# Kernel optimization log

Measured on AMD Instinct MI355X. Metric: run time of the kernel, lower is better.

The kernel has to match this reference:

```python
import jax, jax.numpy as jnp
import numpy as np

B, H, S, F, D = 16, 8, 512, 512, 64
RANK = 12
TOPK_RATIO = 0.1
LN_EPS = 1e-5


def _layernorm(x, w, b):
    mu = jnp.mean(x, axis=-1, keepdims=True)
    var = jnp.mean((x - mu) ** 2, axis=-1, keepdims=True)
    return (x - mu) * jax.lax.rsqrt(var + LN_EPS) * w + b


def _topk_mask(logits, k):
    # keep top-k along last axis, set the rest to -inf (torch topk+scatter equivalent)
    vals, _ = jax.lax.top_k(logits, k)
    kth = vals[..., -1:]
    return jnp.where(logits >= kth, logits, -jnp.inf)


def setup_inputs() -> dict:
    key = jax.random.key(0)
    ks = jax.random.split(key, 4)
    values = jax.random.normal(ks[0], (B, F, H, D), dtype=jnp.float32)
    # stand-in for per-head orthogonal init (rows ~ unit norm scale)
    alpha = jax.random.normal(ks[1], (H, S, F), dtype=jnp.float32) / np.float32(np.sqrt(F))
    temp = jnp.ones((H, 1), dtype=jnp.float32)
    gamma_hs = jnp.zeros((H, S, 1), dtype=jnp.float32)
    U = jax.random.normal(ks[2], (H, S, RANK), dtype=jnp.float32) * 0.01
    V = jax.random.normal(ks[3], (H, RANK, F), dtype=jnp.float32) * 0.01
    ln_w = jnp.ones((F,), dtype=jnp.float32)
    ln_b = jnp.zeros((F,), dtype=jnp.float32)
    return {"values": values, "alpha": alpha, "temp": temp, "gamma_hs": gamma_hs,
            "U": U, "V": V, "ln_w": ln_w, "ln_b": ln_b}


def reference(values, alpha, temp, gamma_hs, U, V, ln_w, ln_b):
    scale = np.float32(1.0 / np.sqrt(F))
    alpha_logits = (alpha * scale)[None]                      # [1,H,S,F]

    # data logits from value energies
    w = jnp.transpose(values, (0, 2, 1, 3))                    # [B,H,F,D]
    energy = jnp.mean(w * w, axis=-1)                          # [B,H,F]
    rms = jnp.maximum(jnp.sqrt(jnp.mean(energy, axis=-1, keepdims=True)), 1e-6)
    score = energy / rms                                       # [B,H,F]
    gain = jax.nn.softplus(temp)[:, 0]                         # [H]
    score = score * gain[None, :, None]
    score = _layernorm(score, ln_w, ln_b)                      # LN over F
    bilinear = jnp.einsum('hsr,hrf->hsf', U, V)                # [H,S,F]
    data_logits = score[:, :, None, :] + gamma_hs[None] + bilinear[None]  # [B,H,S,F]

    k = max(1, int(TOPK_RATIO * F))
    data_logits = _topk_mask(data_logits, k)
    alpha_logits = _topk_mask(alpha_logits, k)

    attn_mix = jax.nn.softmax(data_logits, axis=-1) + jax.nn.softmax(alpha_logits, axis=-1)
    out = jnp.einsum('bhsf,bfhd->bshd', attn_mix, values)      # [B,S,H,D]
    return out
```

## Files before the change

kernel.cpp:

```cpp
#include <hip/hip_runtime.h>
#include <math.h>

#define BB 16
#define HH 8
#define SS 512
#define FF 512
#define DD 64
#define RANKK 12
#define KTOP 51
#define ROWS 8

typedef __attribute__((ext_vector_type(8))) short bf16x8;
typedef __attribute__((ext_vector_type(4))) float f32x4;

__device__ __forceinline__ unsigned short f2bf(float x){
  unsigned u = __float_as_uint(x);
  return (unsigned short)((u + 0x7FFFu + ((u>>16)&1u)) >> 16);
}
__device__ __forceinline__ float bf2f(unsigned short h){
  return __uint_as_float(((unsigned)h)<<16);
}

__device__ __forceinline__ unsigned f2ord(float x){
  unsigned u = __float_as_uint(x);
  return (u & 0x80000000u) ? ~u : (u | 0x80000000u);
}

__device__ __forceinline__ void topk_softmax8(float (&a)[8]){
  unsigned key[8];
#pragma unroll
  for (int j=0;j<8;++j) key[j] = f2ord(a[j]);
  unsigned T = 0u;
#pragma unroll
  for (int bit=31; bit>=0; --bit){
    unsigned Tp = T | (1u<<bit);
    int cnt = 0;
#pragma unroll
    for (int j=0;j<8;++j){
      unsigned long long bl = __ballot(key[j] >= Tp);
      cnt += __popcll(bl);
    }
    if (cnt >= KTOP) T = Tp;
    if (cnt == KTOP) break;
  }
  float m = a[0];
#pragma unroll
  for (int j=1;j<8;++j) m = fmaxf(m, a[j]);
#pragma unroll
  for (int off=32; off>=1; off>>=1) m = fmaxf(m, __shfl_xor(m, off));
  float sum = 0.f;
#pragma unroll
  for (int j=0;j<8;++j){
    float e = (key[j] >= T) ? expf(a[j]-m) : 0.f;
    a[j] = e; sum += e;
  }
#pragma unroll
  for (int off=32; off>=1; off>>=1) sum += __shfl_xor(sum, off);
  float inv = 1.f/sum;
#pragma unroll
  for (int j=0;j<8;++j) a[j] *= inv;
}

__global__ __launch_bounds__(512) void k_prep_all(
    const float* __restrict__ values, const float* __restrict__ temp,
    const float* __restrict__ ln_w, const float* __restrict__ ln_b,
    const float* __restrict__ alpha, float* __restrict__ score_ln,
    unsigned short* __restrict__ hiP, unsigned short* __restrict__ loP,
    float* __restrict__ A_soft)
{
  const int tid = threadIdx.x, w = tid >> 6, lane = tid & 63;
  if (blockIdx.x >= BB*HH){
    const int row = (int)(blockIdx.x - BB*HH) * ROWS + w;
    const float SCALE = (float)(1.0/sqrt((double)FF));
    const float* ar = alpha + (size_t)row*FF + lane*8;
    float4 v0 = *(const float4*)ar;
    float4 v1 = *(const float4*)(ar+4);
    float a[8] = {v0.x*SCALE, v0.y*SCALE, v0.z*SCALE, v0.w*SCALE,
                  v1.x*SCALE, v1.y*SCALE, v1.z*SCALE, v1.w*SCALE};
    topk_softmax8(a);
    float* orow = A_soft + (size_t)row*FF + lane*8;
    *(float4*)orow     = make_float4(a[0],a[1],a[2],a[3]);
    *(float4*)(orow+4) = make_float4(a[4],a[5],a[6],a[7]);
    return;
  }
  __shared__ float tile[64][65];
  __shared__ float s_e[FF];
  __shared__ float ps[8], ps2[8];
  const int b = blockIdx.x / HH, h = blockIdx.x % HH;
  const float* vb = values + ((size_t)b*FF*HH + h)*DD;

  for (int c=0;c<8;++c){
#pragma unroll
    for (int p=0;p<8;++p){
      const int fi = p*8 + w;
      const int f  = c*64 + fi;
      tile[fi][lane] = vb[(size_t)f*HH*DD + lane];
    }
    __syncthreads();
    {
      const int d  = w*8 + (lane>>3);
      const int fj = (lane&7)*8;
      unsigned short hs[8], ls[8];
#pragma unroll
      for (int j=0;j<8;++j){
        float x = tile[fj+j][d];
        hs[j] = f2bf(x);
        ls[j] = f2bf(x - bf2f(hs[j]));
      }
      uint4 H4, L4;
      H4.x=(unsigned)hs[0]|((unsigned)hs[1]<<16); H4.y=(unsigned)hs[2]|((unsigned)hs[3]<<16);
      H4.z=(unsigned)hs[4]|((unsigned)hs[5]<<16); H4.w=(unsigned)hs[6]|((unsigned)hs[7]<<16);
      L4.x=(unsigned)ls[0]|((unsigned)ls[1]<<16); L4.y=(unsigned)ls[2]|((unsigned)ls[3]<<16);
      L4.z=(unsigned)ls[4]|((unsigned)ls[5]<<16); L4.w=(unsigned)ls[6]|((unsigned)ls[7]<<16);
      const size_t base = ((size_t)blockIdx.x*DD + d)*FF + c*64 + fj;
      *(uint4*)(hiP + base) = H4;
      *(uint4*)(loP + base) = L4;
    }
    __syncthreads();
  }

  for (int i=0;i<FF/8;++i){
    int f = w*(FF/8) + i;
    float v = vb[(size_t)f*HH*DD + lane];
    float e = v*v;
#pragma unroll
    for (int off=32; off>=1; off>>=1) e += __shfl_xor(e, off);
    if (lane==0) s_e[f] = e * (1.0f/DD);
  }
  __syncthreads();
  float e = s_e[tid];
  float se = e, se2 = e*e;
#pragma unroll
  for (int off=32; off>=1; off>>=1){ se += __shfl_xor(se, off); se2 += __shfl_xor(se2, off); }
  if (lane==0){ ps[w]=se; ps2[w]=se2; }
  __syncthreads();
  float S1=0.f, S2=0.f;
#pragma unroll
  for (int g=0; g<8; ++g){ S1 += ps[g]; S2 += ps2[g]; }
  float meanE = S1 * (1.0f/FF);
  float rms = fmaxf(sqrtf(meanE), 1e-6f);
  float t = temp[h];
  float gain = (t > 20.f) ? t : log1pf(expf(t));
  float c = gain / rms;
  float mu = c * meanE;
  float var = c*c*(S2*(1.0f/FF) - meanE*meanE);
  float inv = rsqrtf(var + 1e-5f);
  score_ln[(size_t)blockIdx.x*FF + tid] = (c*e - mu)*inv*ln_w[tid] + ln_b[tid];
}

__global__ __launch_bounds__(512) void k_score(const float* __restrict__ values,
    const float* __restrict__ temp, const float* __restrict__ ln_w,
    const float* __restrict__ ln_b, float* __restrict__ score_ln)
{
  const int b = blockIdx.x / HH, h = blockIdx.x % HH;
  const int tid = threadIdx.x, w = tid >> 6, lane = tid & 63;
  __shared__ float s_e[FF];
  __shared__ float ps[8], ps2[8];
  const float* vb = values + ((size_t)b*FF*HH + h)*DD;
  for (int i=0;i<FF/8;++i){
    int f = w*(FF/8) + i;
    float v = vb[(size_t)f*HH*DD + lane];
    float e = v*v;
#pragma unroll
    for (int off=32; off>=1; off>>=1) e += __shfl_xor(e, off);
    if (lane==0) s_e[f] = e * (1.0f/DD);
  }
  __syncthreads();
  float e = s_e[tid];
  float se = e, se2 = e*e;
#pragma unroll
  for (int off=32; off>=1; off>>=1){ se += __shfl_xor(se, off); se2 += __shfl_xor(se2, off); }
  if (lane==0){ ps[w]=se; ps2[w]=se2; }
  __syncthreads();
  float S1=0.f, S2=0.f;
#pragma unroll
  for (int g=0; g<8; ++g){ S1 += ps[g]; S2 += ps2[g]; }
  float meanE = S1 * (1.0f/FF);
  float rms = fmaxf(sqrtf(meanE), 1e-6f);
  float t = temp[h];
  float gain = (t > 20.f) ? t : log1pf(expf(t));
  float c = gain / rms;
  float mu = c * meanE;
  float var = c*c*(S2*(1.0f/FF) - meanE*meanE);
  float inv = rsqrtf(var + 1e-5f);
  score_ln[(size_t)blockIdx.x*FF + tid] = (c*e - mu)*inv*ln_w[tid] + ln_b[tid];
}

__global__ __launch_bounds__(512) void k_alpha(const float* __restrict__ alpha,
                                               float* __restrict__ A_soft)
{
  const int w = threadIdx.x >> 6, lane = threadIdx.x & 63;
  const int row = blockIdx.x * ROWS + w;
  const float SCALE = (float)(1.0/sqrt((double)FF));
  const float* ar = alpha + (size_t)row*FF + lane*8;
  float4 v0 = *(const float4*)ar;
  float4 v1 = *(const float4*)(ar+4);
  float a[8] = {v0.x*SCALE, v0.y*SCALE, v0.z*SCALE, v0.w*SCALE,
                v1.x*SCALE, v1.y*SCALE, v1.z*SCALE, v1.w*SCALE};
  topk_softmax8(a);
  float* orow = A_soft + (size_t)row*FF + lane*8;
  *(float4*)orow     = make_float4(a[0],a[1],a[2],a[3]);
  *(float4*)(orow+4) = make_float4(a[4],a[5],a[6],a[7]);
}

__global__ __launch_bounds__(512) void k_prep_t(const float* __restrict__ values,
    unsigned short* __restrict__ hiP, unsigned short* __restrict__ loP, int b0)
{
  const int bloc_h = blockIdx.x;
  const int b = b0 + bloc_h / HH, h = bloc_h % HH;
  const int tid = threadIdx.x, w = tid >> 6, lane = tid & 63;
  __shared__ float tile[64][65];
  const float* vb = values + ((size_t)b*FF*HH + h)*DD;
  for (int c=0;c<8;++c){
#pragma unroll
    for (int p=0;p<8;++p){
      const int fi = p*8 + w;
      const int f  = c*64 + fi;
      tile[fi][lane] = vb[(size_t)f*HH*DD + lane];
    }
    __syncthreads();
    {
      const int d  = w*8 + (lane>>3);
      const int fj = (lane&7)*8;
      unsigned short hs[8], ls[8];
#pragma unroll
      for (int j=0;j<8;++j){
        float x = tile[fj+j][d];
        hs[j] = f2bf(x);
        ls[j] = f2bf(x - bf2f(hs[j]));
      }
      uint4 H4, L4;
      H4.x=(unsigned)hs[0]|((unsigned)hs[1]<<16); H4.y=(unsigned)hs[2]|((unsigned)hs[3]<<16);
      H4.z=(unsigned)hs[4]|((unsigned)hs[5]<<16); H4.w=(unsigned)hs[6]|((unsigned)hs[7]<<16);
      L4.x=(unsigned)ls[0]|((unsigned)ls[1]<<16); L4.y=(unsigned)ls[2]|((unsigned)ls[3]<<16);
      L4.z=(unsigned)ls[4]|((unsigned)ls[5]<<16); L4.w=(unsigned)ls[6]|((unsigned)ls[7]<<16);
      const size_t base = ((size_t)bloc_h*DD + d)*FF + c*64 + fj;
      *(uint4*)(hiP + base) = H4;
      *(uint4*)(loP + base) = L4;
    }
    __syncthreads();
  }
}

__device__ __forceinline__ void build_mix_row(int bh, int h, int s, int lane,
    const float* __restrict__ score_ln, const float* __restrict__ gamma,
    const float* __restrict__ U, const float* __restrict__ V,
    const float* __restrict__ A_soft, float4& m0, float4& m1)
{
  const int f0 = lane*8;
  const float* sr = score_ln + (size_t)bh*FF + f0;
  float4 sv0 = *(const float4*)sr;
  float4 sv1 = *(const float4*)(sr+4);
  const float g = gamma[h*SS + s];
  float dl[8] = {sv0.x+g, sv0.y+g, sv0.z+g, sv0.w+g,
                 sv1.x+g, sv1.y+g, sv1.z+g, sv1.w+g};
  const float* Ur = U + ((size_t)h*SS + s)*RANKK;
  const float* Vh = V + (size_t)h*RANKK*FF + f0;
#pragma unroll
  for (int r=0;r<RANKK;++r){
    float u = Ur[r];
    float4 b0 = *(const float4*)(Vh + r*FF);
    float4 b1 = *(const float4*)(Vh + r*FF + 4);
    dl[0] += u*b0.x; dl[1] += u*b0.y; dl[2] += u*b0.z; dl[3] += u*b0.w;
    dl[4] += u*b1.x; dl[5] += u*b1.y; dl[6] += u*b1.z; dl[7] += u*b1.w;
  }
  topk_softmax8(dl);
  const float* arow = A_soft + ((size_t)h*SS + s)*FF + f0;
  float4 a0 = *(const float4*)arow;
  float4 a1 = *(const float4*)(arow+4);
  m0 = make_float4(dl[0]+a0.x, dl[1]+a0.y, dl[2]+a0.z, dl[3]+a0.w);
  m1 = make_float4(dl[4]+a1.x, dl[5]+a1.y, dl[6]+a1.z, dl[7]+a1.w);
}

__device__ __forceinline__ void gload16(const void* g, void* l){
  __builtin_amdgcn_global_load_lds(
      (const __attribute__((address_space(1))) unsigned int*)g,
      (__attribute__((address_space(3))) unsigned int*)l, 16, 0, 0);
}

template<int NB>
__global__ __launch_bounds__(512, 4) void k_mfma_t(
    const unsigned short* __restrict__ hiP, const unsigned short* __restrict__ loP,
    const float* __restrict__ gamma, const float* __restrict__ U,
    const float* __restrict__ V, const float* __restrict__ score_ln,
    const float* __restrict__ A_soft, float* __restrict__ out, int b0)
{
  __shared__ __align__(16) unsigned char Abuf[65536];
  __shared__ __align__(16) unsigned char Bbuf[2][8192];
  const int nwg = HH*NB*16;
  const int bid = (blockIdx.x & 7)*(nwg/8) + (blockIdx.x >> 3);
  const int grp  = bid >> 4;
  const int sblk = bid & 15;
  const int h    = grp / NB;
  const int bloc = grp % NB;
  const int b    = b0 + bloc;
  const int s0   = sblk*32;
  const int bh   = b*HH + h;
  const int tid = threadIdx.x, w = tid>>6, lane = tid&63;

  const size_t pbBase = (size_t)(bloc*HH + h)*DD*FF;
  const int dw  = tid >> 3;
  const int s8p = tid & 7;
  const int s8  = s8p ^ (dw & 7);
  const unsigned short* sp = ((s8 & 4) ? loP : hiP)
                             + pbBase + (size_t)dw*FF + (size_t)(s8 & 3)*8;
  gload16(sp, &Bbuf[0][(unsigned)w<<10]);

#pragma unroll
  for (int i=0;i<4;++i){
    const int sl = w*4 + i;
    float4 m0, m1;
    build_mix_row(bh, h, s0+sl, lane, score_ln, gamma, U, V, A_soft, m0, m1);
    float xs[8] = {m0.x,m0.y,m0.z,m0.w,m1.x,m1.y,m1.z,m1.w};
    unsigned short hs[8], ls[8];
#pragma unroll
    for (int j=0;j<8;++j){
      hs[j] = f2bf(xs[j]);
      ls[j] = f2bf(xs[j] - bf2f(hs[j]));
    }
    uint4 H4, L4;
    H4.x = (unsigned)hs[0] | ((unsigned)hs[1]<<16);
    H4.y = (unsigned)hs[2] | ((unsigned)hs[3]<<16);
    H4.z = (unsigned)hs[4] | ((unsigned)hs[5]<<16);
    H4.w = (unsigned)hs[6] | ((unsigned)hs[7]<<16);
    L4.x = (unsigned)ls[0] | ((unsigned)ls[1]<<16);
    L4.y = (unsigned)ls[2] | ((unsigned)ls[3]<<16);
    L4.z = (unsigned)ls[4] | ((unsigned)ls[5]<<16);
    L4.w = (unsigned)ls[6] | ((unsigned)ls[7]<<16);
    const unsigned byt = (unsigned)(sl*1024 + lane*16) ^ (unsigned)((sl&15)<<4);
    *(uint4*)(Abuf + byt)          = H4;
    *(uint4*)(Abuf + 32768 + byt)  = L4;
  }
  __syncthreads();

  const int stile = w>>2, ntile = w&3;
  const int srow  = stile*16 + (lane&15);
  const unsigned sw = (unsigned)((lane&15)<<4);
  const unsigned a0off = (unsigned)(srow*1024 + ((lane>>4)*16));
  const int d    = ntile*16 + (lane&15);
  const int sgr  = lane>>4;
  const unsigned offH = (unsigned)(d*128 + ((sgr    ) ^ (d&7))*16);
  const unsigned offL = (unsigned)(d*128 + ((sgr + 4) ^ (d&7))*16);

  f32x4 acc0 = {0.f,0.f,0.f,0.f};
  f32x4 acc1 = {0.f,0.f,0.f,0.f};

#pragma unroll
  for (int t=0;t<16;++t){
    if (t > 0){
      asm volatile("s_waitcnt vmcnt(0) lgkmcnt(0)" ::: "memory");
      __builtin_amdgcn_s_barrier();
    }
    if (t < 15)
      gload16(sp + (size_t)(t+1)*32, &Bbuf[(t+1)&1][(unsigned)w<<10]);
    const unsigned ax = (a0off + (unsigned)(t*64)) ^ sw;
    bf16x8 ah = *(const bf16x8*)(Abuf + ax);
    bf16x8 al = *(const bf16x8*)(Abuf + 32768 + ax);
    const unsigned char* bb = Bbuf[t&1];
    bf16x8 bhv = *(const bf16x8*)(bb + offH);
    bf16x8 blv = *(const bf16x8*)(bb + offL);
    __builtin_amdgcn_s_setprio(1);
    acc0 = __builtin_amdgcn_mfma_f32_16x16x32_bf16(ah, bhv, acc0, 0, 0, 0);
    acc1 = __builtin_amdgcn_mfma_f32_16x16x32_bf16(al, bhv, acc1, 0, 0, 0);
    acc1 = __builtin_amdgcn_mfma_f32_16x16x32_bf16(ah, blv, acc1, 0, 0, 0);
    __builtin_amdgcn_s_setprio(0);
  }

  const int m0r = stile*16 + (lane>>4)*4;
#pragma unroll
  for (int r=0;r<4;++r){
    const int s = s0 + m0r + r;
    __builtin_nontemporal_store(acc0[r] + acc1[r],
        &out[(((size_t)b*SS + s)*HH + h)*DD + d]);
  }
}

__global__ __launch_bounds__(512) void k_main_lds(const float* __restrict__ values,
    const float* __restrict__ alpha, const float* __restrict__ gamma,
    const float* __restrict__ U, const float* __restrict__ V,
    const float* __restrict__ score_ln, float* __restrict__ out)
{
  const int nwg = BB*HH*(SS/ROWS);
  const int bid = (blockIdx.x & 7)*(nwg/8) + (blockIdx.x >> 3);
  const int blocksPerBH = SS / ROWS;
  const int bh = bid / blocksPerBH;
  const int s0 = (bid % blocksPerBH) * ROWS;
  const int b = bh / HH, h = bh % HH;
  const int tid = threadIdx.x, w = tid >> 6, lane = tid & 63;
  __shared__ float smix[ROWS][FF];

  {
    const int s = s0 + w;
    const int f0 = lane*8;
    const float* sr = score_ln + (size_t)bh*FF + f0;
    float4 sv0 = *(const float4*)sr;
    float4 sv1 = *(const float4*)(sr+4);
    const float g = gamma[h*SS + s];
    float dl[8] = {sv0.x+g, sv0.y+g, sv0.z+g, sv0.w+g,
                   sv1.x+g, sv1.y+g, sv1.z+g, sv1.w+g};
    const float* Ur = U + ((size_t)h*SS + s)*RANKK;
    const float* Vh = V + (size_t)h*RANKK*FF + f0;
#pragma unroll
    for (int r=0;r<RANKK;++r){
      float u = Ur[r];
      float4 b0 = *(const float4*)(Vh + r*FF);
      float4 b1 = *(const float4*)(Vh + r*FF + 4);
      dl[0] += u*b0.x; dl[1] += u*b0.y; dl[2] += u*b0.z; dl[3] += u*b0.w;
      dl[4] += u*b1.x; dl[5] += u*b1.y; dl[6] += u*b1.z; dl[7] += u*b1.w;
    }
    topk_softmax8(dl);
    const float SCALE = (float)(1.0/sqrt((double)FF));
    const float* arow = alpha + ((size_t)h*SS + s)*FF + f0;
    float4 a0 = *(const float4*)arow;
    float4 a1 = *(const float4*)(arow+4);
    float ap[8] = {a0.x*SCALE, a0.y*SCALE, a0.z*SCALE, a0.w*SCALE,
                   a1.x*SCALE, a1.y*SCALE, a1.z*SCALE, a1.w*SCALE};
    topk_softmax8(ap);
    float4 m0 = make_float4(dl[0]+ap[0], dl[1]+ap[1], dl[2]+ap[2], dl[3]+ap[3]);
    float4 m1 = make_float4(dl[4]+ap[4], dl[5]+ap[5], dl[6]+ap[6], dl[7]+ap[7]);
    *(float4*)&smix[w][f0]   = m0;
    *(float4*)&smix[w][f0+4] = m1;
  }
  __syncthreads();

  float acc[ROWS] = {0,0,0,0,0,0,0,0};
  {
    const float* vp = values + (size_t)b*FF*HH*DD + (size_t)h*DD + lane;
#pragma unroll
    for (int i=0;i<16;++i){
      const int f0 = w*64 + i*4;
      float x0 = vp[(size_t)(f0+0)*HH*DD];
      float x1 = vp[(size_t)(f0+1)*HH*DD];
      float x2 = vp[(size_t)(f0+2)*HH*DD];
      float x3 = vp[(size_t)(f0+3)*HH*DD];
#pragma unroll
      for (int r=0;r<ROWS;++r){
        float4 m = *(const float4*)&smix[r][f0];
        acc[r] += m.x*x0 + m.y*x1 + m.z*x2 + m.w*x3;
      }
    }
  }
  __syncthreads();

  float* red = &smix[0][0];
#pragma unroll
  for (int r=0;r<ROWS;++r) red[(w*ROWS + r)*64 + lane] = acc[r];
  __syncthreads();
  {
    const int r = w, dd = lane;
    float sum = 0.f;
#pragma unroll
    for (int g=0; g<8; ++g) sum += red[(g*ROWS + r)*64 + dd];
    out[(((size_t)b*SS + s0 + r)*HH + h)*DD + dd] = sum;
  }
}

extern "C" void kernel_launch(void* const* d_in, const int* in_sizes, int n_in,
                              void* d_out, int out_size, void* d_ws, size_t ws_size,
                              hipStream_t stream) {
  const float* values = (const float*)d_in[0];
  const float* alpha  = (const float*)d_in[1];
  const float* temp   = (const float*)d_in[2];
  const float* gamma  = (const float*)d_in[3];
  const float* U      = (const float*)d_in[4];
  const float* V      = (const float*)d_in[5];
  const float* ln_w   = (const float*)d_in[6];
  const float* ln_b   = (const float*)d_in[7];
  float* out = (float*)d_out;
  float* ws  = (float*)d_ws;

  const size_t scoreN = (size_t)BB*HH*FF;
  const size_t alphaN = (size_t)HH*SS*FF;
  const size_t planeFull = (size_t)BB*HH*DD*FF;
  const size_t planeHalf = planeFull/2;

  float* score_ln = ws;
  float* A_soft   = ws + scoreN;
  unsigned short* hiP = (unsigned short*)(ws + scoreN + alphaN);

  const size_t baseB    = (scoreN + alphaN)*sizeof(float);
  const size_t needFull = baseB + 2*planeFull*sizeof(unsigned short);
  const size_t needHalf = baseB + 2*planeHalf*sizeof(unsigned short);

  if (ws_size >= needFull){
    unsigned short* loP = hiP + planeFull;
    hipLaunchKernelGGL(k_prep_all, dim3(BB*HH + HH*SS/ROWS), dim3(512), 0, stream,
                       values, temp, ln_w, ln_b, alpha, score_ln, hiP, loP, A_soft);
    hipLaunchKernelGGL((k_mfma_t<BB>), dim3(HH*16*BB), dim3(512), 0, stream,
                       hiP, loP, gamma, U, V, score_ln, A_soft, out, 0);
  } else if (ws_size >= needHalf){
    unsigned short* loP = hiP + planeHalf;
    hipLaunchKernelGGL(k_score, dim3(BB*HH), dim3(512), 0, stream,
                       values, temp, ln_w, ln_b, score_ln);
    hipLaunchKernelGGL(k_alpha, dim3(HH*SS/ROWS), dim3(512), 0, stream, alpha, A_soft);
    for (int c=0;c<2;++c){
      hipLaunchKernelGGL(k_prep_t, dim3((BB/2)*HH), dim3(512), 0, stream,
                         values, hiP, loP, c*(BB/2));
      hipLaunchKernelGGL((k_mfma_t<BB/2>), dim3(HH*16*(BB/2)), dim3(512), 0, stream,
                         hiP, loP, gamma, U, V, score_ln, A_soft, out, c*(BB/2));
    }
  } else {
    hipLaunchKernelGGL(k_score, dim3(BB*HH), dim3(512), 0, stream,
                       values, temp, ln_w, ln_b, score_ln);
    hipLaunchKernelGGL(k_main_lds, dim3(BB*HH*(SS/ROWS)), dim3(512), 0, stream,
                       values, alpha, gamma, U, V, score_ln, out);
  }
}
```

Measured before the change: 173.5 us.

## Load MFMA B operands directly from global and stage output through LDS

The double-buffered global_load_lds staging of the hi/lo bf16 B operands is removed, together with its per-iteration waitcnt and barrier. Each lane now loads its 16-byte B fragments straight from global memory, relying on cache reuse across the waves that share a d tile. The output is first written into the now-free A buffer in LDS and then stored as coalesced float4 rows instead of scattered scalar nontemporal stores. This drops the per-step block synchronisation but exposes global load latency inside the MFMA loop and duplicates B reads across waves.

```diff
diff --git a/kernel.cpp b/kernel.cpp
--- a/kernel.cpp
+++ b/kernel.cpp
@@ -272,12 +272,6 @@
   m1 = make_float4(dl[4]+a1.x, dl[5]+a1.y, dl[6]+a1.z, dl[7]+a1.w);
 }
 
-__device__ __forceinline__ void gload16(const void* g, void* l){
-  __builtin_amdgcn_global_load_lds(
-      (const __attribute__((address_space(1))) unsigned int*)g,
-      (__attribute__((address_space(3))) unsigned int*)l, 16, 0, 0);
-}
-
 template<int NB>
 __global__ __launch_bounds__(512, 4) void k_mfma_t(
     const unsigned short* __restrict__ hiP, const unsigned short* __restrict__ loP,
@@ -286,7 +280,6 @@
     const float* __restrict__ A_soft, float* __restrict__ out, int b0)
 {
   __shared__ __align__(16) unsigned char Abuf[65536];
-  __shared__ __align__(16) unsigned char Bbuf[2][8192];
   const int nwg = HH*NB*16;
   const int bid = (blockIdx.x & 7)*(nwg/8) + (blockIdx.x >> 3);
   const int grp  = bid >> 4;
@@ -297,14 +290,6 @@
   const int s0   = sblk*32;
   const int bh   = b*HH + h;
   const int tid = threadIdx.x, w = tid>>6, lane = tid&63;
-
-  const size_t pbBase = (size_t)(bloc*HH + h)*DD*FF;
-  const int dw  = tid >> 3;
-  const int s8p = tid & 7;
-  const int s8  = s8p ^ (dw & 7);
-  const unsigned short* sp = ((s8 & 4) ? loP : hiP)
-                             + pbBase + (size_t)dw*FF + (size_t)(s8 & 3)*8;
-  gload16(sp, &Bbuf[0][(unsigned)w<<10]);
 
 #pragma unroll
   for (int i=0;i<4;++i){
@@ -338,27 +323,22 @@
   const unsigned sw = (unsigned)((lane&15)<<4);
   const unsigned a0off = (unsigned)(srow*1024 + ((lane>>4)*16));
   const int d    = ntile*16 + (lane&15);
-  const int sgr  = lane>>4;
-  const unsigned offH = (unsigned)(d*128 + ((sgr    ) ^ (d&7))*16);
-  const unsigned offL = (unsigned)(d*128 + ((sgr + 4) ^ (d&7))*16);
+  const int frow = (lane>>4)*8;
 
   f32x4 acc0 = {0.f,0.f,0.f,0.f};
   f32x4 acc1 = {0.f,0.f,0.f,0.f};
 
+  const size_t pb = ((size_t)(bloc*HH + h)*DD + d)*FF + frow;
+  const unsigned short* hp = hiP + pb;
+  const unsigned short* lp = loP + pb;
+
 #pragma unroll
   for (int t=0;t<16;++t){
-    if (t > 0){
-      asm volatile("s_waitcnt vmcnt(0) lgkmcnt(0)" ::: "memory");
-      __builtin_amdgcn_s_barrier();
-    }
-    if (t < 15)
-      gload16(sp + (size_t)(t+1)*32, &Bbuf[(t+1)&1][(unsigned)w<<10]);
+    bf16x8 bhv = *(const bf16x8*)(hp + t*32);
+    bf16x8 blv = *(const bf16x8*)(lp + t*32);
     const unsigned ax = (a0off + (unsigned)(t*64)) ^ sw;
     bf16x8 ah = *(const bf16x8*)(Abuf + ax);
     bf16x8 al = *(const bf16x8*)(Abuf + 32768 + ax);
-    const unsigned char* bb = Bbuf[t&1];
-    bf16x8 bhv = *(const bf16x8*)(bb + offH);
-    bf16x8 blv = *(const bf16x8*)(bb + offL);
     __builtin_amdgcn_s_setprio(1);
     acc0 = __builtin_amdgcn_mfma_f32_16x16x32_bf16(ah, bhv, acc0, 0, 0, 0);
     acc1 = __builtin_amdgcn_mfma_f32_16x16x32_bf16(al, bhv, acc1, 0, 0, 0);
@@ -366,12 +346,18 @@
     __builtin_amdgcn_s_setprio(0);
   }
 
+  __syncthreads();
+  float* ob = (float*)Abuf;
   const int m0r = stile*16 + (lane>>4)*4;
 #pragma unroll
-  for (int r=0;r<4;++r){
-    const int s = s0 + m0r + r;
-    __builtin_nontemporal_store(acc0[r] + acc1[r],
-        &out[(((size_t)b*SS + s)*HH + h)*DD + d]);
+  for (int r=0;r<4;++r)
+    ob[(m0r + r)*64 + d] = acc0[r] + acc1[r];
+  __syncthreads();
+  {
+    const int sl = tid >> 4;
+    const int d4 = (tid & 15)*4;
+    const float4 v = *(const float4*)&ob[sl*64 + d4];
+    *(float4*)&out[(((size_t)b*SS + s0 + sl)*HH + h)*DD + d4] = v;
   }
 }
 
```

Result: slower. 191.4 us (+10.3%).

## Split mix construction and MFMA GEMM into software-pipelined fused chunk kernels

Applied to the files above, without the earlier changes.

The main fused kernel is replaced with a two-stage scheme. First the top-k softmax mix matrix is materialised to workspace as bf16 hi/lo planes. A GEMM kernel then reads those planes directly from global memory. Chunks of batches are software-pipelined, so each fused launch computes the mix for chunk c while running the GEMM for chunk c-1, using double-buffered mix storage. This tries to overlap the compute-heavy mix stage with the MFMA stage, at the cost of extra global traffic for the mix planes and a larger workspace requirement.

```diff
diff --git a/kernel.cpp b/kernel.cpp
--- a/kernel.cpp
+++ b/kernel.cpp
@@ -186,62 +186,6 @@
   score_ln[(size_t)blockIdx.x*FF + tid] = (c*e - mu)*inv*ln_w[tid] + ln_b[tid];
 }
 
-__global__ __launch_bounds__(512) void k_alpha(const float* __restrict__ alpha,
-                                               float* __restrict__ A_soft)
-{
-  const int w = threadIdx.x >> 6, lane = threadIdx.x & 63;
-  const int row = blockIdx.x * ROWS + w;
-  const float SCALE = (float)(1.0/sqrt((double)FF));
-  const float* ar = alpha + (size_t)row*FF + lane*8;
-  float4 v0 = *(const float4*)ar;
-  float4 v1 = *(const float4*)(ar+4);
-  float a[8] = {v0.x*SCALE, v0.y*SCALE, v0.z*SCALE, v0.w*SCALE,
-                v1.x*SCALE, v1.y*SCALE, v1.z*SCALE, v1.w*SCALE};
-  topk_softmax8(a);
-  float* orow = A_soft + (size_t)row*FF + lane*8;
-  *(float4*)orow     = make_float4(a[0],a[1],a[2],a[3]);
-  *(float4*)(orow+4) = make_float4(a[4],a[5],a[6],a[7]);
-}
-
-__global__ __launch_bounds__(512) void k_prep_t(const float* __restrict__ values,
-    unsigned short* __restrict__ hiP, unsigned short* __restrict__ loP, int b0)
-{
-  const int bloc_h = blockIdx.x;
-  const int b = b0 + bloc_h / HH, h = bloc_h % HH;
-  const int tid = threadIdx.x, w = tid >> 6, lane = tid & 63;
-  __shared__ float tile[64][65];
-  const float* vb = values + ((size_t)b*FF*HH + h)*DD;
-  for (int c=0;c<8;++c){
-#pragma unroll
-    for (int p=0;p<8;++p){
-      const int fi = p*8 + w;
-      const int f  = c*64 + fi;
-      tile[fi][lane] = vb[(size_t)f*HH*DD + lane];
-    }
-    __syncthreads();
-    {
-      const int d  = w*8 + (lane>>3);
-      const int fj = (lane&7)*8;
-      unsigned short hs[8], ls[8];
-#pragma unroll
-      for (int j=0;j<8;++j){
-        float x = tile[fj+j][d];
-        hs[j] = f2bf(x);
-        ls[j] = f2bf(x - bf2f(hs[j]));
-      }
-      uint4 H4, L4;
-      H4.x=(unsigned)hs[0]|((unsigned)hs[1]<<16); H4.y=(unsigned)hs[2]|((unsigned)hs[3]<<16);
-      H4.z=(unsigned)hs[4]|((unsigned)hs[5]<<16); H4.w=(unsigned)hs[6]|((unsigned)hs[7]<<16);
-      L4.x=(unsigned)ls[0]|((unsigned)ls[1]<<16); L4.y=(unsigned)ls[2]|((unsigned)ls[3]<<16);
-      L4.z=(unsigned)ls[4]|((unsigned)ls[5]<<16); L4.w=(unsigned)ls[6]|((unsigned)ls[7]<<16);
-      const size_t base = ((size_t)bloc_h*DD + d)*FF + c*64 + fj;
-      *(uint4*)(hiP + base) = H4;
-      *(uint4*)(loP + base) = L4;
-    }
-    __syncthreads();
-  }
-}
-
 __device__ __forceinline__ void build_mix_row(int bh, int h, int s, int lane,
     const float* __restrict__ score_ln, const float* __restrict__ gamma,
     const float* __restrict__ U, const float* __restrict__ V,
@@ -270,6 +214,140 @@
   float4 a1 = *(const float4*)(arow+4);
   m0 = make_float4(dl[0]+a0.x, dl[1]+a0.y, dl[2]+a0.z, dl[3]+a0.w);
   m1 = make_float4(dl[4]+a1.x, dl[5]+a1.y, dl[6]+a1.z, dl[7]+a1.w);
+}
+
+template<int NBC>
+__device__ __forceinline__ void mix_body(int bid, const float* __restrict__ gamma,
+    const float* __restrict__ U, const float* __restrict__ V,
+    const float* __restrict__ score_ln, const float* __restrict__ A_soft,
+    unsigned short* __restrict__ mixH, unsigned short* __restrict__ mixL,
+    int b0, int tid)
+{
+  const int w = tid>>6, lane = tid&63;
+  const int rid = bid*8 + w;
+  const int bi  = rid % NBC;
+  const int hs  = rid / NBC;
+  const int h   = hs >> 9;
+  const int s   = hs & 511;
+  float4 m0, m1;
+  build_mix_row((b0+bi)*HH + h, h, s, lane, score_ln, gamma, U, V, A_soft, m0, m1);
+  float xs[8] = {m0.x,m0.y,m0.z,m0.w,m1.x,m1.y,m1.z,m1.w};
+  unsigned short hv[8], lv[8];
+#pragma unroll
+  for (int j=0;j<8;++j){
+    hv[j] = f2bf(xs[j]);
+    lv[j] = f2bf(xs[j] - bf2f(hv[j]));
+  }
+  uint4 H4, L4;
+  H4.x=(unsigned)hv[0]|((unsigned)hv[1]<<16); H4.y=(unsigned)hv[2]|((unsigned)hv[3]<<16);
+  H4.z=(unsigned)hv[4]|((unsigned)hv[5]<<16); H4.w=(unsigned)hv[6]|((unsigned)hv[7]<<16);
+  L4.x=(unsigned)lv[0]|((unsigned)lv[1]<<16); L4.y=(unsigned)lv[2]|((unsigned)lv[3]<<16);
+  L4.z=(unsigned)lv[4]|((unsigned)lv[5]<<16); L4.w=(unsigned)lv[6]|((unsigned)lv[7]<<16);
+  const size_t base = ((size_t)(bi*HH + h)*SS + s)*FF + lane*8;
+  *(uint4*)(mixH + base) = H4;
+  *(uint4*)(mixL + base) = L4;
+}
+
+template<int NBC>
+__device__ __forceinline__ void gemm_body(int bid,
+    const unsigned short* __restrict__ mixH, const unsigned short* __restrict__ mixL,
+    const unsigned short* __restrict__ hiP, const unsigned short* __restrict__ loP,
+    float* __restrict__ out, int b0, float* lds, int tid)
+{
+  const int stile = bid & 3;
+  const int g  = bid >> 2;
+  const int h  = g / NBC;
+  const int bi = g % NBC;
+  const int b  = b0 + bi;
+  const int s0 = stile*128;
+  const int w = tid>>6, lane = tid&63;
+  const int fr = (lane>>4)*8;
+
+  const size_t abase = ((size_t)(bi*HH + h)*SS + s0 + w*16 + (lane&15))*FF + fr;
+  const unsigned short* mh = mixH + abase;
+  const unsigned short* ml = mixL + abase;
+  const size_t bbase = ((size_t)(b*HH + h)*DD + (lane&15))*FF + fr;
+  const unsigned short* bh0 = hiP + bbase;
+  const unsigned short* bl0 = loP + bbase;
+
+  f32x4 c0[4] = {{0,0,0,0},{0,0,0,0},{0,0,0,0},{0,0,0,0}};
+  f32x4 c1[4] = {{0,0,0,0},{0,0,0,0},{0,0,0,0},{0,0,0,0}};
+
+#pragma unroll
+  for (int t=0;t<16;++t){
+    bf16x8 ah = *(const bf16x8*)(mh + t*32);
+    bf16x8 al = *(const bf16x8*)(ml + t*32);
+#pragma unroll
+    for (int nt=0;nt<4;++nt){
+      bf16x8 bhv = *(const bf16x8*)(bh0 + (size_t)nt*16*FF + t*32);
+      bf16x8 blv = *(const bf16x8*)(bl0 + (size_t)nt*16*FF + t*32);
+      c0[nt] = __builtin_amdgcn_mfma_f32_16x16x32_bf16(ah, bhv, c0[nt], 0, 0, 0);
+      c1[nt] = __builtin_amdgcn_mfma_f32_16x16x32_bf16(al, bhv, c1[nt], 0, 0, 0);
+      c1[nt] = __builtin_amdgcn_mfma_f32_16x16x32_bf16(ah, blv, c1[nt], 0, 0, 0);
+    }
+  }
+
+  const int m0r = (lane>>4)*4;
+#pragma unroll
+  for (int nt=0;nt<4;++nt){
+    const int d = nt*16 + (lane&15);
+#pragma unroll
+    for (int r=0;r<4;++r)
+      lds[(w*16 + m0r + r)*64 + d] = c0[nt][r] + c1[nt][r];
+  }
+  __syncthreads();
+#pragma unroll
+  for (int p=0;p<4;++p){
+    const int row = p*32 + (tid>>4);
+    const int col = (tid&15)*4;
+    *(float4*)&out[(((size_t)b*SS + s0 + row)*HH + h)*DD + col]
+        = *(const float4*)&lds[row*64 + col];
+  }
+}
+
+template<int NBC>
+__global__ __launch_bounds__(512, 4) void k_mix(const float* __restrict__ gamma,
+    const float* __restrict__ U, const float* __restrict__ V,
+    const float* __restrict__ score_ln, const float* __restrict__ A_soft,
+    unsigned short* __restrict__ mixH, unsigned short* __restrict__ mixL, int b0)
+{
+  const int nwg = NBC*HH*SS/8;
+  const int bid = (blockIdx.x & 7)*(nwg/8) + (blockIdx.x >> 3);
+  mix_body<NBC>(bid, gamma, U, V, score_ln, A_soft, mixH, mixL, b0, threadIdx.x);
+}
+
+template<int NBC>
+__global__ __launch_bounds__(512, 3) void k_gemm(
+    const unsigned short* __restrict__ mixH, const unsigned short* __restrict__ mixL,
+    const unsigned short* __restrict__ hiP, const unsigned short* __restrict__ loP,
+    float* __restrict__ out, int b0)
+{
+  __shared__ float lds[128*64];
+  const int NC = NBC*32;
+  const int bid = (blockIdx.x & 7)*(NC/8) + (blockIdx.x >> 3);
+  gemm_body<NBC>(bid, mixH, mixL, hiP, loP, out, b0, lds, threadIdx.x);
+}
+
+template<int NBC>
+__global__ __launch_bounds__(512, 3) void k_fused(const float* __restrict__ gamma,
+    const float* __restrict__ U, const float* __restrict__ V,
+    const float* __restrict__ score_ln, const float* __restrict__ A_soft,
+    unsigned short* __restrict__ mixHw, unsigned short* __restrict__ mixLw, int b0p,
+    const unsigned short* __restrict__ mixHr, const unsigned short* __restrict__ mixLr,
+    int b0c, const unsigned short* __restrict__ hiP, const unsigned short* __restrict__ loP,
+    float* __restrict__ out)
+{
+  __shared__ float lds[128*64];
+  const int NC = NBC*32;
+  if ((int)blockIdx.x < NC){
+    const int bid = (blockIdx.x & 7)*(NC/8) + (blockIdx.x >> 3);
+    gemm_body<NBC>(bid, mixHr, mixLr, hiP, loP, out, b0c, lds, threadIdx.x);
+  } else {
+    const int pidx = blockIdx.x - NC;
+    const int NP = NBC*HH*SS/8;
+    const int bid = (pidx & 7)*(NP/8) + (pidx >> 3);
+    mix_body<NBC>(bid, gamma, U, V, score_ln, A_soft, mixHw, mixLw, b0p, threadIdx.x);
+  }
 }
 
 __device__ __forceinline__ void gload16(const void* g, void* l){
@@ -312,21 +390,17 @@
     float4 m0, m1;
     build_mix_row(bh, h, s0+sl, lane, score_ln, gamma, U, V, A_soft, m0, m1);
     float xs[8] = {m0.x,m0.y,m0.z,m0.w,m1.x,m1.y,m1.z,m1.w};
-    unsigned short hs[8], ls[8];
+    unsigned short hv[8], lv[8];
 #pragma unroll
     for (int j=0;j<8;++j){
-      hs[j] = f2bf(xs[j]);
-      ls[j] = f2bf(xs[j] - bf2f(hs[j]));
+      hv[j] = f2bf(xs[j]);
+      lv[j] = f2bf(xs[j] - bf2f(hv[j]));
     }
     uint4 H4, L4;
-    H4.x = (unsigned)hs[0] | ((unsigned)hs[1]<<16);
-    H4.y = (unsigned)hs[2] | ((unsigned)hs[3]<<16);
-    H4.z = (unsigned)hs[4] | ((unsigned)hs[5]<<16);
-    H4.w = (unsigned)hs[6] | ((unsigned)hs[7]<<16);
-    L4.x = (unsigned)ls[0] | ((unsigned)ls[1]<<16);
-    L4.y = (unsigned)ls[2] | ((unsigned)ls[3]<<16);
-    L4.z = (unsigned)ls[4] | ((unsigned)ls[5]<<16);
-    L4.w = (unsigned)ls[6] | ((unsigned)ls[7]<<16);
+    H4.x=(unsigned)hv[0]|((unsigned)hv[1]<<16); H4.y=(unsigned)hv[2]|((unsigned)hv[3]<<16);
+    H4.z=(unsigned)hv[4]|((unsigned)hv[5]<<16); H4.w=(unsigned)hv[6]|((unsigned)hv[7]<<16);
+    L4.x=(unsigned)lv[0]|((unsigned)lv[1]<<16); L4.y=(unsigned)lv[2]|((unsigned)lv[3]<<16);
+    L4.z=(unsigned)lv[4]|((unsigned)lv[5]<<16); L4.w=(unsigned)lv[6]|((unsigned)lv[7]<<16);
     const unsigned byt = (unsigned)(sl*1024 + lane*16) ^ (unsigned)((sl&15)<<4);
     *(uint4*)(Abuf + byt)          = H4;
     *(uint4*)(Abuf + 32768 + byt)  = L4;
@@ -455,6 +529,29 @@
   }
 }
 
+template<int NBC>
+static void launch_paired(const float* gamma, const float* U, const float* V,
+    float* score_ln, float* A_soft, unsigned short* hiP, unsigned short* loP,
+    unsigned short* mixBase, float* out, hipStream_t stream)
+{
+  const int nch = BB/NBC;
+  const size_t mixE = (size_t)NBC*HH*SS*FF;
+  unsigned short* mH[2] = {mixBase,              mixBase + 2*mixE};
+  unsigned short* mL[2] = {mixBase + mixE,       mixBase + 3*mixE};
+  const int NP = NBC*HH*SS/8, NC = NBC*32;
+
+  hipLaunchKernelGGL((k_mix<NBC>), dim3(NP), dim3(512), 0, stream,
+                     gamma, U, V, score_ln, A_soft, mH[0], mL[0], 0);
+  for (int c=1; c<nch; ++c){
+    hipLaunchKernelGGL((k_fused<NBC>), dim3(NC+NP), dim3(512), 0, stream,
+                       gamma, U, V, score_ln, A_soft,
+                       mH[c&1], mL[c&1], c*NBC,
+                       mH[(c-1)&1], mL[(c-1)&1], (c-1)*NBC, hiP, loP, out);
+  }
+  hipLaunchKernelGGL((k_gemm<NBC>), dim3(NC), dim3(512), 0, stream,
+                     mH[(nch-1)&1], mL[(nch-1)&1], hiP, loP, out, (nch-1)*NBC);
+}
+
 extern "C" void kernel_launch(void* const* d_in, const int* in_sizes, int n_in,
                               void* d_out, int out_size, void* d_ws, size_t ws_size,
                               hipStream_t stream) {
@@ -471,34 +568,43 @@
 
   const size_t scoreN = (size_t)BB*HH*FF;
   const size_t alphaN = (size_t)HH*SS*FF;
-  const size_t planeFull = (size_t)BB*HH*DD*FF;
-  const size_t planeHalf = planeFull/2;
+  const size_t planeN = (size_t)BB*HH*DD*FF;
 
   float* score_ln = ws;
   float* A_soft   = ws + scoreN;
   unsigned short* hiP = (unsigned short*)(ws + scoreN + alphaN);
-
-  const size_t baseB    = (scoreN + alphaN)*sizeof(float);
-  const size_t needFull = baseB + 2*planeFull*sizeof(unsigned short);
-  const size_t needHalf = baseB + 2*planeHalf*sizeof(unsigned short);
-
-  if (ws_size >= needFull){
-    unsigned short* loP = hiP + planeFull;
+  unsigned short* loP = hiP + planeN;
+  unsigned short* mixBase = loP + planeN;
+
+  const size_t baseB = scoreN*4 + alphaN*4 + 2*planeN*2;
+  auto needP = [&](int nbc)->size_t{ return baseB + (size_t)nbc*4*HH*SS*FF*2; };
+  const size_t needS1 = baseB + (size_t)2*HH*SS*FF*2;
+
+  if (ws_size >= needS1){
+    hipLaunchKernelGGL(k_prep_all, dim3(BB*HH + HH*SS/ROWS), dim3(512), 0, stream,
+                       values, temp, ln_w, ln_b, alpha, score_ln, hiP, loP, A_soft);
+    if (ws_size >= needP(4)){
+      launch_paired<4>(gamma, U, V, score_ln, A_soft, hiP, loP, mixBase, out, stream);
+    } else if (ws_size >= needP(2)){
+      launch_paired<2>(gamma, U, V, score_ln, A_soft, hiP, loP, mixBase, out, stream);
+    } else if (ws_size >= needP(1)){
+      launch_paired<1>(gamma, U, V, score_ln, A_soft, hiP, loP, mixBase, out, stream);
+    } else {
+      const size_t mixE = (size_t)HH*SS*FF;
+      unsigned short* mH = mixBase;
+      unsigned short* mL = mixBase + mixE;
+      for (int c=0;c<BB;++c){
+        hipLaunchKernelGGL((k_mix<1>), dim3(HH*SS/8), dim3(512), 0, stream,
+                           gamma, U, V, score_ln, A_soft, mH, mL, c);
+        hipLaunchKernelGGL((k_gemm<1>), dim3(32), dim3(512), 0, stream,
+                           mH, mL, hiP, loP, out, c);
+      }
+    }
+  } else if (ws_size >= baseB){
     hipLaunchKernelGGL(k_prep_all, dim3(BB*HH + HH*SS/ROWS), dim3(512), 0, stream,
                        values, temp, ln_w, ln_b, alpha, score_ln, hiP, loP, A_soft);
     hipLaunchKernelGGL((k_mfma_t<BB>), dim3(HH*16*BB), dim3(512), 0, stream,
                        hiP, loP, gamma, U, V, score_ln, A_soft, out, 0);
-  } else if (ws_size >= needHalf){
-    unsigned short* loP = hiP + planeHalf;
-    hipLaunchKernelGGL(k_score, dim3(BB*HH), dim3(512), 0, stream,
-                       values, temp, ln_w, ln_b, score_ln);
-    hipLaunchKernelGGL(k_alpha, dim3(HH*SS/ROWS), dim3(512), 0, stream, alpha, A_soft);
-    for (int c=0;c<2;++c){
-      hipLaunchKernelGGL(k_prep_t, dim3((BB/2)*HH), dim3(512), 0, stream,
-                         values, hiP, loP, c*(BB/2));
-      hipLaunchKernelGGL((k_mfma_t<BB/2>), dim3(HH*16*(BB/2)), dim3(512), 0, stream,
-                         hiP, loP, gamma, U, V, score_ln, A_soft, out, c*(BB/2));
-    }
   } else {
     hipLaunchKernelGGL(k_score, dim3(BB*HH), dim3(512), 0, stream,
                        values, temp, ln_w, ln_b, score_ln);
```

New measurement: 240.2 us. 38.5% more time.

## Fuse energy reduction into transpose pass and stage MFMA output through LDS

Applied to the files above, without the earlier changes.

In the prep kernel, the per-feature energy reduction is computed from the values already loaded for the bf16 hi/lo transpose, which removes a second full read of values and an extra barrier. In the MFMA kernel, accumulator results are first written to LDS and then stored to global memory as coalesced float4 rows instead of scattered scalar nontemporal stores. The half-workspace fallback path and its helper kernels are removed. This adds two barriers and LDS reuse of the A buffer at the end of the MFMA kernel.

```diff
diff --git a/kernel.cpp b/kernel.cpp
--- a/kernel.cpp
+++ b/kernel.cpp
@@ -94,7 +94,12 @@
     for (int p=0;p<8;++p){
       const int fi = p*8 + w;
       const int f  = c*64 + fi;
-      tile[fi][lane] = vb[(size_t)f*HH*DD + lane];
+      float v = vb[(size_t)f*HH*DD + lane];
+      tile[fi][lane] = v;
+      float e = v*v;
+#pragma unroll
+      for (int off=32; off>=1; off>>=1) e += __shfl_xor(e, off);
+      if (lane==0) s_e[f] = e * (1.0f/DD);
     }
     __syncthreads();
     {
@@ -119,15 +124,6 @@
     __syncthreads();
   }
 
-  for (int i=0;i<FF/8;++i){
-    int f = w*(FF/8) + i;
-    float v = vb[(size_t)f*HH*DD + lane];
-    float e = v*v;
-#pragma unroll
-    for (int off=32; off>=1; off>>=1) e += __shfl_xor(e, off);
-    if (lane==0) s_e[f] = e * (1.0f/DD);
-  }
-  __syncthreads();
   float e = s_e[tid];
   float se = e, se2 = e*e;
 #pragma unroll
@@ -184,62 +180,6 @@
   float var = c*c*(S2*(1.0f/FF) - meanE*meanE);
   float inv = rsqrtf(var + 1e-5f);
   score_ln[(size_t)blockIdx.x*FF + tid] = (c*e - mu)*inv*ln_w[tid] + ln_b[tid];
-}
-
-__global__ __launch_bounds__(512) void k_alpha(const float* __restrict__ alpha,
-                                               float* __restrict__ A_soft)
-{
-  const int w = threadIdx.x >> 6, lane = threadIdx.x & 63;
-  const int row = blockIdx.x * ROWS + w;
-  const float SCALE = (float)(1.0/sqrt((double)FF));
-  const float* ar = alpha + (size_t)row*FF + lane*8;
-  float4 v0 = *(const float4*)ar;
-  float4 v1 = *(const float4*)(ar+4);
-  float a[8] = {v0.x*SCALE, v0.y*SCALE, v0.z*SCALE, v0.w*SCALE,
-                v1.x*SCALE, v1.y*SCALE, v1.z*SCALE, v1.w*SCALE};
-  topk_softmax8(a);
-  float* orow = A_soft + (size_t)row*FF + lane*8;
-  *(float4*)orow     = make_float4(a[0],a[1],a[2],a[3]);
-  *(float4*)(orow+4) = make_float4(a[4],a[5],a[6],a[7]);
-}
-
-__global__ __launch_bounds__(512) void k_prep_t(const float* __restrict__ values,
-    unsigned short* __restrict__ hiP, unsigned short* __restrict__ loP, int b0)
-{
-  const int bloc_h = blockIdx.x;
-  const int b = b0 + bloc_h / HH, h = bloc_h % HH;
-  const int tid = threadIdx.x, w = tid >> 6, lane = tid & 63;
-  __shared__ float tile[64][65];
-  const float* vb = values + ((size_t)b*FF*HH + h)*DD;
-  for (int c=0;c<8;++c){
-#pragma unroll
-    for (int p=0;p<8;++p){
-      const int fi = p*8 + w;
-      const int f  = c*64 + fi;
-      tile[fi][lane] = vb[(size_t)f*HH*DD + lane];
-    }
-    __syncthreads();
-    {
-      const int d  = w*8 + (lane>>3);
-      const int fj = (lane&7)*8;
-      unsigned short hs[8], ls[8];
-#pragma unroll
-      for (int j=0;j<8;++j){
-        float x = tile[fj+j][d];
-        hs[j] = f2bf(x);
-        ls[j] = f2bf(x - bf2f(hs[j]));
-      }
-      uint4 H4, L4;
-      H4.x=(unsigned)hs[0]|((unsigned)hs[1]<<16); H4.y=(unsigned)hs[2]|((unsigned)hs[3]<<16);
-      H4.z=(unsigned)hs[4]|((unsigned)hs[5]<<16); H4.w=(unsigned)hs[6]|((unsigned)hs[7]<<16);
-      L4.x=(unsigned)ls[0]|((unsigned)ls[1]<<16); L4.y=(unsigned)ls[2]|((unsigned)ls[3]<<16);
-      L4.z=(unsigned)ls[4]|((unsigned)ls[5]<<16); L4.w=(unsigned)ls[6]|((unsigned)ls[7]<<16);
-      const size_t base = ((size_t)bloc_h*DD + d)*FF + c*64 + fj;
-      *(uint4*)(hiP + base) = H4;
-      *(uint4*)(loP + base) = L4;
-    }
-    __syncthreads();
-  }
 }
 
 __device__ __forceinline__ void build_mix_row(int bh, int h, int s, int lane,
@@ -312,21 +252,17 @@
     float4 m0, m1;
     build_mix_row(bh, h, s0+sl, lane, score_ln, gamma, U, V, A_soft, m0, m1);
     float xs[8] = {m0.x,m0.y,m0.z,m0.w,m1.x,m1.y,m1.z,m1.w};
-    unsigned short hs[8], ls[8];
+    unsigned short hv[8], lv[8];
 #pragma unroll
     for (int j=0;j<8;++j){
-      hs[j] = f2bf(xs[j]);
-      ls[j] = f2bf(xs[j] - bf2f(hs[j]));
+      hv[j] = f2bf(xs[j]);
+      lv[j] = f2bf(xs[j] - bf2f(hv[j]));
     }
     uint4 H4, L4;
-    H4.x = (unsigned)hs[0] | ((unsigned)hs[1]<<16);
-    H4.y = (unsigned)hs[2] | ((unsigned)hs[3]<<16);
-    H4.z = (unsigned)hs[4] | ((unsigned)hs[5]<<16);
-    H4.w = (unsigned)hs[6] | ((unsigned)hs[7]<<16);
-    L4.x = (unsigned)ls[0] | ((unsigned)ls[1]<<16);
-    L4.y = (unsigned)ls[2] | ((unsigned)ls[3]<<16);
-    L4.z = (unsigned)ls[4] | ((unsigned)ls[5]<<16);
-    L4.w = (unsigned)ls[6] | ((unsigned)ls[7]<<16);
+    H4.x=(unsigned)hv[0]|((unsigned)hv[1]<<16); H4.y=(unsigned)hv[2]|((unsigned)hv[3]<<16);
+    H4.z=(unsigned)hv[4]|((unsigned)hv[5]<<16); H4.w=(unsigned)hv[6]|((unsigned)hv[7]<<16);
+    L4.x=(unsigned)lv[0]|((unsigned)lv[1]<<16); L4.y=(unsigned)lv[2]|((unsigned)lv[3]<<16);
+    L4.z=(unsigned)lv[4]|((unsigned)lv[5]<<16); L4.w=(unsigned)lv[6]|((unsigned)lv[7]<<16);
     const unsigned byt = (unsigned)(sl*1024 + lane*16) ^ (unsigned)((sl&15)<<4);
     *(uint4*)(Abuf + byt)          = H4;
     *(uint4*)(Abuf + 32768 + byt)  = L4;
@@ -366,12 +302,18 @@
     __builtin_amdgcn_s_setprio(0);
   }
 
+  __syncthreads();
+  float* ob = (float*)Abuf;
   const int m0r = stile*16 + (lane>>4)*4;
 #pragma unroll
-  for (int r=0;r<4;++r){
-    const int s = s0 + m0r + r;
-    __builtin_nontemporal_store(acc0[r] + acc1[r],
-        &out[(((size_t)b*SS + s)*HH + h)*DD + d]);
+  for (int r=0;r<4;++r)
+    ob[(m0r + r)*64 + d] = acc0[r] + acc1[r];
+  __syncthreads();
+  {
+    const int row = tid >> 4;
+    const int col = (tid & 15)*4;
+    *(float4*)&out[(((size_t)b*SS + s0 + row)*HH + h)*DD + col]
+        = *(const float4*)&ob[row*64 + col];
   }
 }
 
@@ -471,34 +413,20 @@
 
   const size_t scoreN = (size_t)BB*HH*FF;
   const size_t alphaN = (size_t)HH*SS*FF;
-  const size_t planeFull = (size_t)BB*HH*DD*FF;
-  const size_t planeHalf = planeFull/2;
+  const size_t planeN = (size_t)BB*HH*DD*FF;
 
   float* score_ln = ws;
   float* A_soft   = ws + scoreN;
   unsigned short* hiP = (unsigned short*)(ws + scoreN + alphaN);
-
-  const size_t baseB    = (scoreN + alphaN)*sizeof(float);
-  const size_t needFull = baseB + 2*planeFull*sizeof(unsigned short);
-  const size_t needHalf = baseB + 2*planeHalf*sizeof(unsigned short);
+  unsigned short* loP = hiP + planeN;
+
+  const size_t needFull = scoreN*4 + alphaN*4 + 2*planeN*2;
 
   if (ws_size >= needFull){
-    unsigned short* loP = hiP + planeFull;
     hipLaunchKernelGGL(k_prep_all, dim3(BB*HH + HH*SS/ROWS), dim3(512), 0, stream,
                        values, temp, ln_w, ln_b, alpha, score_ln, hiP, loP, A_soft);
     hipLaunchKernelGGL((k_mfma_t<BB>), dim3(HH*16*BB), dim3(512), 0, stream,
                        hiP, loP, gamma, U, V, score_ln, A_soft, out, 0);
-  } else if (ws_size >= needHalf){
-    unsigned short* loP = hiP + planeHalf;
-    hipLaunchKernelGGL(k_score, dim3(BB*HH), dim3(512), 0, stream,
-                       values, temp, ln_w, ln_b, score_ln);
-    hipLaunchKernelGGL(k_alpha, dim3(HH*SS/ROWS), dim3(512), 0, stream, alpha, A_soft);
-    for (int c=0;c<2;++c){
-      hipLaunchKernelGGL(k_prep_t, dim3((BB/2)*HH), dim3(512), 0, stream,
-                         values, hiP, loP, c*(BB/2));
-      hipLaunchKernelGGL((k_mfma_t<BB/2>), dim3(HH*16*(BB/2)), dim3(512), 0, stream,
-                         hiP, loP, gamma, U, V, score_ln, A_soft, out, c*(BB/2));
-    }
   } else {
     hipLaunchKernelGGL(k_score, dim3(BB*HH), dim3(512), 0, stream,
                        values, temp, ln_w, ln_b, score_ln);
```

Result: no change. 176.6 us (+1.8%).
